# Kernel tuning notes

Hardware: AMD Instinct MI355X
Metric: run time of the kernel (lower is better)

The kernel has to match this reference:

```python
import jax, jax.numpy as jnp
import numpy as np

MODES = 16
WIDTH = 64
SCHMIDT = 8
N_LAYERS = 4


def _spectral_conv(x, wr, wi, modes):
    """Quantum spectral conv: truncated 2D FFT -> complex Schmidt-rank einsum -> inverse FFT.
    x: (B,H,W,C) real. wr, wi: (modes,modes,C,C,S)."""
    b, H, W, C = x.shape
    S = wr.shape[-1]
    # quantum_fourier_modes: keep low (modes x modes) Fourier modes
    x_ft = jnp.fft.fftn(x, axes=(1, 2))[:, :modes, :modes, :]          # (B,m,n,C) complex
    w = wr + 1j * wi                                                     # (m,n,C,C,S)
    # tensor_product_einsum('b...nc,mncos->b...mos')
    out_ft = jnp.einsum('bxnc,mncos->bxmos', x_ft, w)                   # (B,m,m,C,S)
    # recombine Schmidt components (normalized sum over rank)
    out_ft = out_ft.sum(axis=-1) * (1.0 / float(np.sqrt(S)))            # (B,m,m,C)
    full = jnp.zeros((b, H, W, C), dtype=x_ft.dtype).at[:, :modes, :modes, :].set(out_ft)
    # inverse quantum_fourier_modes + .real
    return jnp.fft.ifftn(full, axes=(1, 2)).real


def setup_inputs() -> dict:
    key = jax.random.key(0)
    ks = jax.random.split(key, 12)
    B, H, W, Cin = 16, 128, 128, 3
    sc = 0.02
    inp = {
        'x': jax.random.normal(ks[0], (B, H, W, Cin), jnp.float32),
        'fc_in_w': jax.random.normal(ks[1], (Cin, WIDTH), jnp.float32) * sc,
        'fc_in_b': jnp.zeros((WIDTH,), jnp.float32),
        'wr': jax.random.normal(ks[2], (N_LAYERS, MODES, MODES, WIDTH, WIDTH, SCHMIDT), jnp.float32) * sc,
        'wi': jax.random.normal(ks[3], (N_LAYERS, MODES, MODES, WIDTH, WIDTH, SCHMIDT), jnp.float32) * sc,
        'ww': jax.random.normal(ks[4], (N_LAYERS, WIDTH, WIDTH), jnp.float32) * sc,
        'wb': jnp.zeros((N_LAYERS, WIDTH), jnp.float32),
        'fc1_w': jax.random.normal(ks[5], (WIDTH, 128), jnp.float32) * sc,
        'fc1_b': jnp.zeros((128,), jnp.float32),
        'fc2_w': jax.random.normal(ks[6], (128, 1), jnp.float32) * sc,
        'fc2_b': jnp.zeros((1,), jnp.float32),
    }
    return inp


def reference(x, fc_in_w, fc_in_b, wr, wi, ww, wb, fc1_w, fc1_b, fc2_w, fc2_b) -> jnp.ndarray:
    h = x @ fc_in_w + fc_in_b                                   # (B,H,W,width)
    for i in range(N_LAYERS):
        x1 = _spectral_conv(h, wr[i], wi[i], MODES)             # quantum spectral path
        x2 = h @ ww[i] + wb[i]                                  # pointwise Dense path
        h = jax.nn.gelu(x1 + x2)
    h = jax.nn.gelu(h @ fc1_w + fc1_b)
    return h @ fc2_w + fc2_b                                    # (B,H,W,1)
```

## Files before the change

### kernel.cpp

```cpp
#include <hip/hip_runtime.h>
#include <math.h>


#define TWO_PI_128 0.049087385212340517f

__device__ __forceinline__ float gelu_f(float v) {
  float ex = 1.5957691216057308f * v * fmaf(0.044715f, v * v, 1.0f);
  float e = __expf(fminf(ex, 30.0f));
  float r = __builtin_amdgcn_rcpf(e + 1.0f);
  return fmaf(-v, r, v);
}

__global__ __launch_bounds__(256) void k_fc_in(const float* __restrict__ x,
    const float* __restrict__ w, const float* __restrict__ b,
    float* __restrict__ h) {
  int t = blockIdx.x * 256 + threadIdx.x;
  int pix = t >> 4, c4 = (t & 15) << 2;
  float x0 = x[pix * 3], x1 = x[pix * 3 + 1], x2 = x[pix * 3 + 2];
  float4 acc = *(const float4*)&b[c4];
  float4 w0 = *(const float4*)&w[c4];
  float4 w1 = *(const float4*)&w[64 + c4];
  float4 w2 = *(const float4*)&w[128 + c4];
  acc.x = fmaf(x2, w2.x, fmaf(x1, w1.x, fmaf(x0, w0.x, acc.x)));
  acc.y = fmaf(x2, w2.y, fmaf(x1, w1.y, fmaf(x0, w0.y, acc.y)));
  acc.z = fmaf(x2, w2.z, fmaf(x1, w1.z, fmaf(x0, w0.z, acc.z)));
  acc.w = fmaf(x2, w2.w, fmaf(x1, w1.w, fmaf(x0, w0.w, acc.w)));
  *(float4*)&h[(size_t)pix * 64 + c4] = acc;
}

__global__ __launch_bounds__(256) void k_prep(const float* __restrict__ wr,
    const float* __restrict__ wi, float* __restrict__ Br, float* __restrict__ Bi) {
  int t = blockIdx.x * 256 + threadIdx.x;
  int o = t & 63, c = (t >> 6) & 63, n = (t >> 12) & 15, m = t >> 16;
  const float4* pr = (const float4*)(wr) + (size_t)t * 2;
  float4 a = pr[0], d = pr[1];
  float sr = ((a.x + a.y) + (a.z + a.w)) + ((d.x + d.y) + (d.z + d.w));
  const float4* pi = (const float4*)(wi) + (size_t)t * 2;
  a = pi[0]; d = pi[1];
  float si = ((a.x + a.y) + (a.z + a.w)) + ((d.x + d.y) + (d.z + d.w));
  const float scale = 0.35355339059327373f / 16384.0f;
  int k = n * 64 + c, j = m * 64 + o;
  Br[k * 1024 + j] = sr * scale;
  Bi[k * 1024 + j] = si * scale;
}

__global__ __launch_bounds__(256) void k_dft_y(const float* __restrict__ h,
                                               float2* __restrict__ A1) {
  __shared__ float sh[128 * 64];
  int bx = blockIdx.x;
  const float* src = h + (size_t)bx * 8192;
  for (int i = threadIdx.x; i < 2048; i += 256)
    *(float4*)&sh[i * 4] = *(const float4*)&src[i * 4];
  __syncthreads();
  int c = threadIdx.x & 63, kg = threadIdx.x >> 6;
  float s4r[4][4], s4i[4][4];
  float w4r[4], w4i[4], c4t[4], s4t[4];
  #pragma unroll
  for (int q = 0; q < 4; ++q) {
    int ky = kg + 4 * q;
    __sincosf(-TWO_PI_128 * 4.0f * (float)ky, &s4t[q], &c4t[q]);
    w4r[q] = 1.f; w4i[q] = 0.f;
    #pragma unroll
    for (int p = 0; p < 4; ++p) { s4r[q][p] = 0.f; s4i[q][p] = 0.f; }
  }
  for (int m = 0; m < 32; ++m) {
    float hv[4];
    #pragma unroll
    for (int p = 0; p < 4; ++p) hv[p] = sh[(4 * m + p) * 64 + c];
    #pragma unroll
    for (int q = 0; q < 4; ++q) {
      #pragma unroll
      for (int p = 0; p < 4; ++p) {
        s4r[q][p] = fmaf(hv[p], w4r[q], s4r[q][p]);
        s4i[q][p] = fmaf(hv[p], w4i[q], s4i[q][p]);
      }
      float nw = w4r[q] * c4t[q] - w4i[q] * s4t[q];
      w4i[q] = fmaf(w4i[q], c4t[q], w4r[q] * s4t[q]);
      w4r[q] = nw;
    }
  }
  #pragma unroll
  for (int q = 0; q < 4; ++q) {
    int ky = kg + 4 * q;
    float s1, c1;
    __sincosf(-TWO_PI_128 * (float)ky, &s1, &c1);
    float sr = s4r[q][0], si = s4i[q][0];
    float wr_ = c1, wi_ = s1;
    #pragma unroll
    for (int p = 1; p < 4; ++p) {
      sr = fmaf(s4r[q][p], wr_, sr); sr = fmaf(-s4i[q][p], wi_, sr);
      si = fmaf(s4r[q][p], wi_, si); si = fmaf(s4i[q][p], wr_, si);
      float nw = wr_ * c1 - wi_ * s1;
      wi_ = fmaf(wi_, c1, wr_ * s1);
      wr_ = nw;
    }
    A1[((size_t)bx * 16 + ky) * 64 + c] = make_float2(sr, si);
  }
}

__global__ __launch_bounds__(256) void k_dft_x(const float2* __restrict__ A1,
    float* __restrict__ Ar, float* __restrict__ Ai) {
  __shared__ float2 sh[128 * 32];
  int b = blockIdx.x, ky = blockIdx.y, ch = blockIdx.z;
  int c0 = ch * 32;
  for (int i = threadIdx.x; i < 2048; i += 256) {
    int xx = i >> 4, u = (i & 15) * 2;
    *(float4*)&sh[xx * 32 + u] =
        *(const float4*)&A1[(((size_t)b * 128 + xx) * 16 + ky) * 64 + c0 + u];
  }
  __syncthreads();
  int cl = threadIdx.x & 31, kxg = threadIdx.x >> 5;
  float cs[2], sn[2], wr_[2], wi_[2], sr[2], si[2];
  #pragma unroll
  for (int q = 0; q < 2; ++q) {
    int kx = kxg + 8 * q;
    __sincosf(-TWO_PI_128 * (float)kx, &sn[q], &cs[q]);
    wr_[q] = 1.f; wi_[q] = 0.f; sr[q] = 0.f; si[q] = 0.f;
  }
  for (int xx = 0; xx < 128; ++xx) {
    float2 v = sh[xx * 32 + cl];
    #pragma unroll
    for (int q = 0; q < 2; ++q) {
      sr[q] = fmaf(v.x, wr_[q], sr[q]); sr[q] = fmaf(-v.y, wi_[q], sr[q]);
      si[q] = fmaf(v.x, wi_[q], si[q]); si[q] = fmaf(v.y, wr_[q], si[q]);
      float nw = wr_[q] * cs[q] - wi_[q] * sn[q];
      wi_[q] = fmaf(wi_[q], cs[q], wr_[q] * sn[q]);
      wr_[q] = nw;
    }
  }
  #pragma unroll
  for (int q = 0; q < 2; ++q) {
    int kx = kxg + 8 * q;
    int row = b * 16 + kx, col = ky * 64 + c0 + cl;
    Ar[row * 1024 + col] = sr[q];
    Ai[row * 1024 + col] = si[q];
  }
}

#define CMAC(cr, ci, ax, ay, bx, by)                 \
  cr = fmaf(ax, bx, cr); cr = fmaf(-(ay), by, cr);   \
  ci = fmaf(ax, by, ci); ci = fmaf(ay, bx, ci);

__global__ __launch_bounds__(256) void k_gemm(const float* __restrict__ Ar,
    const float* __restrict__ Ai, const float* __restrict__ Br,
    const float* __restrict__ Bi, float2* __restrict__ Cp,
    float2* __restrict__ Pp) {
  __shared__ float2 As[2][64][34];
  __shared__ float2 Bs[2][32][66];
  int t = threadIdx.x;
  int tx = t & 15, ty = t >> 4;
  int col0 = blockIdx.x * 64, row0 = blockIdx.y * 64, kb0 = blockIdx.z * 128;
  int ra = t >> 2, ka8 = (t & 3) * 8;
  int rb = t >> 3, jb8 = (t & 7) * 8;
  float4 arv0, arv1, aiv0, aiv1, brv0, brv1, biv0, biv1;
  float cr[4][4] = {{0,0,0,0},{0,0,0,0},{0,0,0,0},{0,0,0,0}};
  float ci[4][4] = {{0,0,0,0},{0,0,0,0},{0,0,0,0},{0,0,0,0}};

  auto ldT = [&](int k0) {
    int g = (row0 + ra) * 1024 + k0 + ka8;
    arv0 = *(const float4*)&Ar[g]; arv1 = *(const float4*)&Ar[g + 4];
    aiv0 = *(const float4*)&Ai[g]; aiv1 = *(const float4*)&Ai[g + 4];
    int gb = (k0 + rb) * 1024 + col0 + jb8;
    brv0 = *(const float4*)&Br[gb]; brv1 = *(const float4*)&Br[gb + 4];
    biv0 = *(const float4*)&Bi[gb]; biv1 = *(const float4*)&Bi[gb + 4];
  };
  auto stT = [&](int buf) {
    *(float4*)&As[buf][ra][ka8]     = make_float4(arv0.x, aiv0.x, arv0.y, aiv0.y);
    *(float4*)&As[buf][ra][ka8 + 2] = make_float4(arv0.z, aiv0.z, arv0.w, aiv0.w);
    *(float4*)&As[buf][ra][ka8 + 4] = make_float4(arv1.x, aiv1.x, arv1.y, aiv1.y);
    *(float4*)&As[buf][ra][ka8 + 6] = make_float4(arv1.z, aiv1.z, arv1.w, aiv1.w);
    *(float4*)&Bs[buf][rb][jb8]     = make_float4(brv0.x, biv0.x, brv0.y, biv0.y);
    *(float4*)&Bs[buf][rb][jb8 + 2] = make_float4(brv0.z, biv0.z, brv0.w, biv0.w);
    *(float4*)&Bs[buf][rb][jb8 + 4] = make_float4(brv1.x, biv1.x, brv1.y, biv1.y);
    *(float4*)&Bs[buf][rb][jb8 + 6] = make_float4(brv1.z, biv1.z, brv1.w, biv1.w);
  };

  ldT(kb0); stT(0);
  __syncthreads();
  for (int kt = 0; kt < 4; ++kt) {
    if (kt < 3) ldT(kb0 + (kt + 1) * 32);
    int cur = kt & 1;
    #pragma unroll 4
    for (int kk2 = 0; kk2 < 16; ++kk2) {
      float4 av[4];
      #pragma unroll
      for (int rr = 0; rr < 4; ++rr)
        av[rr] = *(const float4*)&As[cur][ty * 4 + rr][kk2 * 2];
      float2 b0[4], b1[4];
      #pragma unroll
      for (int jj = 0; jj < 4; ++jj) b0[jj] = Bs[cur][kk2 * 2][tx + jj * 16];
      #pragma unroll
      for (int jj = 0; jj < 4; ++jj) b1[jj] = Bs[cur][kk2 * 2 + 1][tx + jj * 16];
      #pragma unroll
      for (int rr = 0; rr < 4; ++rr) {
        #pragma unroll
        for (int jj = 0; jj < 4; ++jj) {
          CMAC(cr[rr][jj], ci[rr][jj], av[rr].x, av[rr].y, b0[jj].x, b0[jj].y)
          CMAC(cr[rr][jj], ci[rr][jj], av[rr].z, av[rr].w, b1[jj].x, b1[jj].y)
        }
      }
    }
    if (kt < 3) stT(cur ^ 1);
    __syncthreads();
  }
  float2* Co = (blockIdx.z == 0) ? Cp : Pp + (size_t)(blockIdx.z - 1) * 262144;
  #pragma unroll
  for (int rr = 0; rr < 4; ++rr) {
    int r = row0 + ty * 4 + rr;
    #pragma unroll
    for (int jj = 0; jj < 4; ++jj) {
      int j = col0 + tx + jj * 16;
      Co[(size_t)r * 1024 + j] = make_float2(cr[rr][jj], ci[rr][jj]);
    }
  }
}

__global__ __launch_bounds__(256) void k_csum(float2* __restrict__ Cp,
                                              const float2* __restrict__ Pp) {
  int i = blockIdx.x * 256 + threadIdx.x;
  float4* c0 = (float4*)Cp;
  float4 s = c0[i];
  #pragma unroll
  for (int z = 0; z < 7; ++z) {
    float4 v = ((const float4*)(Pp + (size_t)z * 262144))[i];
    s.x += v.x; s.y += v.y; s.z += v.z; s.w += v.w;
  }
  c0[i] = s;
}

__global__ __launch_bounds__(256) void k_ifft_y(const float2* __restrict__ Cp,
                                                float2* __restrict__ T) {
  __shared__ float2 Cl[1024];
  int b = blockIdx.x >> 4, kx = blockIdx.x & 15;
  int row = b * 16 + kx;
  for (int i = threadIdx.x; i < 512; i += 256)
    *(float4*)&Cl[i * 2] = *(const float4*)&Cp[(size_t)row * 1024 + i * 2];
  __syncthreads();
  int c = threadIdx.x & 63, yg = threadIdx.x >> 6;
  for (int y = yg; y < 128; y += 4) {
    float snv, csv;
    __sincosf(TWO_PI_128 * (float)y, &snv, &csv);
    float wr_ = 1.f, wi_ = 0.f, sr = 0.f, si = 0.f;
    #pragma unroll
    for (int ky = 0; ky < 16; ++ky) {
      float2 v = Cl[ky * 64 + c];
      sr = fmaf(v.x, wr_, sr); sr = fmaf(-v.y, wi_, sr);
      si = fmaf(v.x, wi_, si); si = fmaf(v.y, wr_, si);
      float nw = wr_ * csv - wi_ * snv;
      wi_ = fmaf(wi_, csv, wr_ * snv);
      wr_ = nw;
    }
    T[(((size_t)b * 128 + y) * 16 + kx) * 64 + c] = make_float2(sr, si);
  }
}

__global__ __launch_bounds__(256, 4) void k_layer_out(const float* hin,
    const float2* __restrict__ T, const float* __restrict__ ww,
    const float* __restrict__ wb, float* hout) {
  __shared__ alignas(16) float wwT[64 * 68];
  __shared__ alignas(16) float2 Tl[1024];
  int b = blockIdx.x >> 7, y = blockIdx.x & 127;
  for (int i = threadIdx.x; i < 1024; i += 256) {
    int k = i >> 4, c4 = (i & 15) << 2;
    float4 v = *(const float4*)&ww[k * 64 + c4];
    wwT[(c4 + 0) * 68 + k] = v.x;
    wwT[(c4 + 1) * 68 + k] = v.y;
    wwT[(c4 + 2) * 68 + k] = v.z;
    wwT[(c4 + 3) * 68 + k] = v.w;
  }
  const float2* Tp = T + ((size_t)b * 128 + y) * 1024;
  for (int i = threadIdx.x; i < 512; i += 256)
    *(float4*)&Tl[i * 2] = *(const float4*)&Tp[i * 2];
  __syncthreads();
  int ct = threadIdx.x & 7, xg = threadIdx.x >> 3;
  float acc[4][8];
  #pragma unroll
  for (int cc = 0; cc < 8; ++cc) {
    float bv = wb[ct + 8 * cc];
    #pragma unroll
    for (int j = 0; j < 4; ++j) acc[j][cc] = bv;
  }
  #pragma unroll
  for (int kx = 0; kx < 16; ++kx) {
    float tr[8], ti[8];
    #pragma unroll
    for (int cc = 0; cc < 8; ++cc) {
      float2 v = Tl[kx * 64 + ct + 8 * cc];
      tr[cc] = v.x; ti[cc] = v.y;
    }
    float s0v, c0v;
    __sincosf(TWO_PI_128 * (float)(kx * xg), &s0v, &c0v);
    float wr_ = c0v, wi_ = s0v;
    #pragma unroll
    for (int j = 0; j < 4; ++j) {
      #pragma unroll
      for (int cc = 0; cc < 8; ++cc) {
        acc[j][cc] = fmaf(tr[cc], wr_, acc[j][cc]);
        acc[j][cc] = fmaf(-ti[cc], wi_, acc[j][cc]);
      }
      float owr = wr_, owi = wi_;
      if ((kx & 3) == 1)      { wr_ = -owi; wi_ =  owr; }
      else if ((kx & 3) == 2) { wr_ = -owr; wi_ = -owi; }
      else if ((kx & 3) == 3) { wr_ =  owi; wi_ = -owr; }
    }
  }
  const float* hp = hin + (((size_t)b * 128 + xg) * 128 + y) * 64;
  #pragma unroll 1
  for (int kq = 0; kq < 64; kq += 4) {
    float4 wv[8];
    #pragma unroll
    for (int cc = 0; cc < 8; ++cc)
      wv[cc] = *(const float4*)&wwT[(ct + 8 * cc) * 68 + kq];
    #pragma unroll
    for (int j = 0; j < 4; ++j) {
      float4 hv = *(const float4*)&hp[(size_t)j * 262144 + kq];
      #pragma unroll
      for (int cc = 0; cc < 8; ++cc) {
        acc[j][cc] = fmaf(hv.x, wv[cc].x, acc[j][cc]);
        acc[j][cc] = fmaf(hv.y, wv[cc].y, acc[j][cc]);
        acc[j][cc] = fmaf(hv.z, wv[cc].z, acc[j][cc]);
        acc[j][cc] = fmaf(hv.w, wv[cc].w, acc[j][cc]);
      }
    }
  }
  __syncthreads();
  #pragma unroll
  for (int j = 0; j < 4; ++j) {
    int xx = xg + 32 * j;
    size_t base = (((size_t)b * 128 + xx) * 128 + y) * 64 + ct;
    #pragma unroll
    for (int cc = 0; cc < 8; ++cc)
      hout[base + 8 * cc] = gelu_f(acc[j][cc]);
  }
}

__global__ __launch_bounds__(256) void k_final(const float* __restrict__ h,
    const float* __restrict__ w1, const float* __restrict__ b1,
    const float* __restrict__ w2, const float* __restrict__ b2,
    float* __restrict__ out) {
  __shared__ alignas(16) float w1T[128 * 68];
  __shared__ alignas(16) float hl[128 * 68];
  __shared__ float b1s[128];
  __shared__ float w2s[128];
  for (int i = threadIdx.x; i < 8192; i += 256) {
    int k = i >> 7, j = i & 127;
    w1T[j * 68 + k] = w1[i];
  }
  if (threadIdx.x < 128) {
    b1s[threadIdx.x] = b1[threadIdx.x];
    w2s[threadIdx.x] = w2[threadIdx.x];
  }
  int r0 = blockIdx.x * 128;
  for (int i = threadIdx.x; i < 2048; i += 256) {
    int r = i >> 4, kq = (i & 15) * 4;
    float4 v = *(const float4*)&h[(size_t)(r0 + r) * 64 + kq];
    *(float4*)&hl[r * 68 + kq] = v;
  }
  __syncthreads();
  int jt = threadIdx.x & 15, rg = threadIdx.x >> 4;
  float acc[8][8];
  #pragma unroll
  for (int cc = 0; cc < 8; ++cc) {
    float bv = b1s[jt + 16 * cc];
    #pragma unroll
    for (int ii = 0; ii < 8; ++ii) acc[ii][cc] = bv;
  }
  #pragma unroll 1
  for (int kq = 0; kq < 64; kq += 4) {
    float4 hv[8];
    #pragma unroll
    for (int ii = 0; ii < 8; ++ii)
      hv[ii] = *(const float4*)&hl[(rg + 16 * ii) * 68 + kq];
    #pragma unroll
    for (int cc = 0; cc < 8; ++cc) {
      float4 wv = *(const float4*)&w1T[(jt + 16 * cc) * 68 + kq];
      #pragma unroll
      for (int ii = 0; ii < 8; ++ii) {
        acc[ii][cc] = fmaf(hv[ii].x, wv.x, acc[ii][cc]);
        acc[ii][cc] = fmaf(hv[ii].y, wv.y, acc[ii][cc]);
        acc[ii][cc] = fmaf(hv[ii].z, wv.z, acc[ii][cc]);
        acc[ii][cc] = fmaf(hv[ii].w, wv.w, acc[ii][cc]);
      }
    }
  }
  float b2v = b2[0];
  #pragma unroll
  for (int ii = 0; ii < 8; ++ii) {
    float part = 0.f;
    #pragma unroll
    for (int cc = 0; cc < 8; ++cc)
      part = fmaf(gelu_f(acc[ii][cc]), w2s[jt + 16 * cc], part);
    part += __shfl_xor(part, 1, 64);
    part += __shfl_xor(part, 2, 64);
    part += __shfl_xor(part, 4, 64);
    part += __shfl_xor(part, 8, 64);
    if (jt == 0) out[r0 + rg + 16 * ii] = part + b2v;
  }
}

extern "C" void kernel_launch(void* const* d_in, const int* in_sizes, int n_in,
                              void* d_out, int out_size, void* d_ws, size_t ws_size,
                              hipStream_t stream) {
  (void)in_sizes; (void)n_in; (void)out_size; (void)ws_size;
  const float* x      = (const float*)d_in[0];
  const float* fcin_w = (const float*)d_in[1];
  const float* fcin_b = (const float*)d_in[2];
  const float* wr     = (const float*)d_in[3];
  const float* wi     = (const float*)d_in[4];
  const float* ww     = (const float*)d_in[5];
  const float* wb     = (const float*)d_in[6];
  const float* fc1_w  = (const float*)d_in[7];
  const float* fc1_b  = (const float*)d_in[8];
  const float* fc2_w  = (const float*)d_in[9];
  const float* fc2_b  = (const float*)d_in[10];
  float* out = (float*)d_out;

  float*  hA = (float*)d_ws;
  float2* A1 = (float2*)(hA + 16777216);
  float*  Ar = (float*)(A1 + 2097152);
  float*  Ai = Ar + 262144;
  float*  Br = Ai + 262144;
  float*  Bi = Br + 1048576;
  float2* Cp = (float2*)(Bi + 1048576);

  k_fc_in<<<16384, 256, 0, stream>>>(x, fcin_w, fcin_b, hA);
  for (int l = 0; l < 4; ++l) {
    k_prep<<<4096, 256, 0, stream>>>(wr + (size_t)l * 8388608,
                                     wi + (size_t)l * 8388608, Br, Bi);
    k_dft_y<<<2048, 256, 0, stream>>>(hA, A1);
    k_dft_x<<<dim3(16, 16, 2), 256, 0, stream>>>(A1, Ar, Ai);
    k_gemm<<<dim3(16, 4, 8), 256, 0, stream>>>(Ar, Ai, Br, Bi, Cp, A1);
    k_csum<<<512, 256, 0, stream>>>(Cp, A1);
    k_ifft_y<<<256, 256, 0, stream>>>(Cp, A1);
    k_layer_out<<<2048, 256, 0, stream>>>(hA, A1, ww + (size_t)l * 4096,
                                          wb + (size_t)l * 64, hA);
  }
  k_final<<<2048, 256, 0, stream>>>(hA, fc1_w, fc1_b, fc2_w, fc2_b, out);
}
```

Before: 964.5 us.

## Replace FP32 complex GEMM with split-bf16 MFMA GEMM and fold partial sum

Replaces the FP32 CUDA-core complex GEMM with an MFMA bf16 GEMM. Each operand is split into high and low bf16 parts, and three products per real product are kept to approximate fp32 accuracy. New split kernels convert A and B into an MFMA-friendly packed layout. The split-K is reduced from 8 to 2, and the remaining partial sum moves into the ifft_y load, which removes the csum kernel. This adds conversion passes and extra memory traffic in exchange, and it loses some precision compared with full fp32.

```diff
diff --git a/kernel.cpp b/kernel.cpp
--- a/kernel.cpp
+++ b/kernel.cpp
@@ -3,12 +3,22 @@
 
 
 #define TWO_PI_128 0.049087385212340517f
+
+typedef __attribute__((ext_vector_type(8))) short bf16x8;
+typedef __attribute__((ext_vector_type(4))) float f32x4;
 
 __device__ __forceinline__ float gelu_f(float v) {
   float ex = 1.5957691216057308f * v * fmaf(0.044715f, v * v, 1.0f);
   float e = __expf(fminf(ex, 30.0f));
   float r = __builtin_amdgcn_rcpf(e + 1.0f);
   return fmaf(-v, r, v);
+}
+
+__device__ __forceinline__ ushort bf16_rne(float v, float& back) {
+  uint u = __float_as_uint(v);
+  uint r = (u + 0x7FFFu + ((u >> 16) & 1u)) >> 16;
+  back = __uint_as_float(r << 16);
+  return (ushort)r;
 }
 
 __global__ __launch_bounds__(256) void k_fc_in(const float* __restrict__ x,
@@ -137,104 +147,118 @@
   }
 }
 
-#define CMAC(cr, ci, ax, ay, bx, by)                 \
-  cr = fmaf(ax, bx, cr); cr = fmaf(-(ay), by, cr);   \
-  ci = fmaf(ax, by, ci); ci = fmaf(ay, bx, ci);
-
-__global__ __launch_bounds__(256) void k_gemm(const float* __restrict__ Ar,
-    const float* __restrict__ Ai, const float* __restrict__ Br,
-    const float* __restrict__ Bi, float2* __restrict__ Cp,
-    float2* __restrict__ Pp) {
-  __shared__ float2 As[2][64][34];
-  __shared__ float2 Bs[2][32][66];
-  int t = threadIdx.x;
-  int tx = t & 15, ty = t >> 4;
-  int col0 = blockIdx.x * 64, row0 = blockIdx.y * 64, kb0 = blockIdx.z * 128;
-  int ra = t >> 2, ka8 = (t & 3) * 8;
-  int rb = t >> 3, jb8 = (t & 7) * 8;
-  float4 arv0, arv1, aiv0, aiv1, brv0, brv1, biv0, biv1;
-  float cr[4][4] = {{0,0,0,0},{0,0,0,0},{0,0,0,0},{0,0,0,0}};
-  float ci[4][4] = {{0,0,0,0},{0,0,0,0},{0,0,0,0},{0,0,0,0}};
-
-  auto ldT = [&](int k0) {
-    int g = (row0 + ra) * 1024 + k0 + ka8;
-    arv0 = *(const float4*)&Ar[g]; arv1 = *(const float4*)&Ar[g + 4];
-    aiv0 = *(const float4*)&Ai[g]; aiv1 = *(const float4*)&Ai[g + 4];
-    int gb = (k0 + rb) * 1024 + col0 + jb8;
-    brv0 = *(const float4*)&Br[gb]; brv1 = *(const float4*)&Br[gb + 4];
-    biv0 = *(const float4*)&Bi[gb]; biv1 = *(const float4*)&Bi[gb + 4];
+__global__ __launch_bounds__(256) void k_asplit(const float* __restrict__ Ar,
+    const float* __restrict__ Ai, ushort* __restrict__ Ap) {
+  int g = blockIdx.x * 256 + threadIdx.x;
+  size_t off = (size_t)g * 8;
+  float4 r0 = *(const float4*)&Ar[off], r1 = *(const float4*)&Ar[off + 4];
+  float4 i0 = *(const float4*)&Ai[off], i1 = *(const float4*)&Ai[off + 4];
+  float vr[8] = {r0.x, r0.y, r0.z, r0.w, r1.x, r1.y, r1.z, r1.w};
+  float vi[8] = {i0.x, i0.y, i0.z, i0.w, i1.x, i1.y, i1.z, i1.w};
+  ushort hr[8], lr[8], hi_[8], li[8];
+  #pragma unroll
+  for (int j = 0; j < 8; ++j) {
+    float back, d;
+    hr[j] = bf16_rne(vr[j], back);
+    lr[j] = bf16_rne(vr[j] - back, d);
+    hi_[j] = bf16_rne(vi[j], back);
+    li[j] = bf16_rne(vi[j] - back, d);
+  }
+  auto pack = [](const ushort* s) {
+    return make_uint4((uint)s[0] | ((uint)s[1] << 16), (uint)s[2] | ((uint)s[3] << 16),
+                      (uint)s[4] | ((uint)s[5] << 16), (uint)s[6] | ((uint)s[7] << 16));
   };
-  auto stT = [&](int buf) {
-    *(float4*)&As[buf][ra][ka8]     = make_float4(arv0.x, aiv0.x, arv0.y, aiv0.y);
-    *(float4*)&As[buf][ra][ka8 + 2] = make_float4(arv0.z, aiv0.z, arv0.w, aiv0.w);
-    *(float4*)&As[buf][ra][ka8 + 4] = make_float4(arv1.x, aiv1.x, arv1.y, aiv1.y);
-    *(float4*)&As[buf][ra][ka8 + 6] = make_float4(arv1.z, aiv1.z, arv1.w, aiv1.w);
-    *(float4*)&Bs[buf][rb][jb8]     = make_float4(brv0.x, biv0.x, brv0.y, biv0.y);
-    *(float4*)&Bs[buf][rb][jb8 + 2] = make_float4(brv0.z, biv0.z, brv0.w, biv0.w);
-    *(float4*)&Bs[buf][rb][jb8 + 4] = make_float4(brv1.x, biv1.x, brv1.y, biv1.y);
-    *(float4*)&Bs[buf][rb][jb8 + 6] = make_float4(brv1.z, biv1.z, brv1.w, biv1.w);
+  *(uint4*)(Ap + 0 * 262144 + off) = pack(hr);
+  *(uint4*)(Ap + 1 * 262144 + off) = pack(lr);
+  *(uint4*)(Ap + 2 * 262144 + off) = pack(hi_);
+  *(uint4*)(Ap + 3 * 262144 + off) = pack(li);
+}
+
+__global__ __launch_bounds__(256) void k_bsplit(const float* __restrict__ Br,
+    const float* __restrict__ Bi, ushort* __restrict__ Bf) {
+  int t = blockIdx.x * 256 + threadIdx.x;
+  int l = t & 63, ks = (t >> 6) & 31, nt = t >> 11;
+  int col = nt * 16 + (l & 15);
+  int kb = ks * 32 + (l >> 4) * 8;
+  ushort hr[8], lr[8], hi_[8], li[8];
+  #pragma unroll
+  for (int j = 0; j < 8; ++j) {
+    float vr = Br[(size_t)(kb + j) * 1024 + col];
+    float vi = Bi[(size_t)(kb + j) * 1024 + col];
+    float back, d;
+    hr[j] = bf16_rne(vr, back);
+    lr[j] = bf16_rne(vr - back, d);
+    hi_[j] = bf16_rne(vi, back);
+    li[j] = bf16_rne(vi - back, d);
+  }
+  auto pack = [](const ushort* s) {
+    return make_uint4((uint)s[0] | ((uint)s[1] << 16), (uint)s[2] | ((uint)s[3] << 16),
+                      (uint)s[4] | ((uint)s[5] << 16), (uint)s[6] | ((uint)s[7] << 16));
   };
-
-  ldT(kb0); stT(0);
-  __syncthreads();
-  for (int kt = 0; kt < 4; ++kt) {
-    if (kt < 3) ldT(kb0 + (kt + 1) * 32);
-    int cur = kt & 1;
-    #pragma unroll 4
-    for (int kk2 = 0; kk2 < 16; ++kk2) {
-      float4 av[4];
-      #pragma unroll
-      for (int rr = 0; rr < 4; ++rr)
-        av[rr] = *(const float4*)&As[cur][ty * 4 + rr][kk2 * 2];
-      float2 b0[4], b1[4];
-      #pragma unroll
-      for (int jj = 0; jj < 4; ++jj) b0[jj] = Bs[cur][kk2 * 2][tx + jj * 16];
-      #pragma unroll
-      for (int jj = 0; jj < 4; ++jj) b1[jj] = Bs[cur][kk2 * 2 + 1][tx + jj * 16];
-      #pragma unroll
-      for (int rr = 0; rr < 4; ++rr) {
-        #pragma unroll
-        for (int jj = 0; jj < 4; ++jj) {
-          CMAC(cr[rr][jj], ci[rr][jj], av[rr].x, av[rr].y, b0[jj].x, b0[jj].y)
-          CMAC(cr[rr][jj], ci[rr][jj], av[rr].z, av[rr].w, b1[jj].x, b1[jj].y)
-        }
-      }
-    }
-    if (kt < 3) stT(cur ^ 1);
-    __syncthreads();
-  }
-  float2* Co = (blockIdx.z == 0) ? Cp : Pp + (size_t)(blockIdx.z - 1) * 262144;
-  #pragma unroll
-  for (int rr = 0; rr < 4; ++rr) {
-    int r = row0 + ty * 4 + rr;
-    #pragma unroll
-    for (int jj = 0; jj < 4; ++jj) {
-      int j = col0 + tx + jj * 16;
-      Co[(size_t)r * 1024 + j] = make_float2(cr[rr][jj], ci[rr][jj]);
-    }
-  }
-}
-
-__global__ __launch_bounds__(256) void k_csum(float2* __restrict__ Cp,
-                                              const float2* __restrict__ Pp) {
-  int i = blockIdx.x * 256 + threadIdx.x;
-  float4* c0 = (float4*)Cp;
-  float4 s = c0[i];
-  #pragma unroll
-  for (int z = 0; z < 7; ++z) {
-    float4 v = ((const float4*)(Pp + (size_t)z * 262144))[i];
-    s.x += v.x; s.y += v.y; s.z += v.z; s.w += v.w;
-  }
-  c0[i] = s;
+  size_t off = (size_t)t * 8;
+  *(uint4*)(Bf + 0 * 1048576 + off) = pack(hr);
+  *(uint4*)(Bf + 1 * 1048576 + off) = pack(lr);
+  *(uint4*)(Bf + 2 * 1048576 + off) = pack(hi_);
+  *(uint4*)(Bf + 3 * 1048576 + off) = pack(li);
+}
+
+__global__ __launch_bounds__(256) void k_gemm_mfma(const ushort* __restrict__ Ap,
+    const ushort* __restrict__ Bf, float2* __restrict__ Cp,
+    float2* __restrict__ Pz1) {
+  int wid = threadIdx.x >> 6, l = threadIdx.x & 63;
+  int bid = blockIdx.x;
+  int z = bid & 1;
+  int tile = (bid >> 1) * 4 + wid;
+  int tr = tile & 15, tc = tile >> 4;
+  int r0 = tr * 16;
+  int lr = l & 15, lk = l >> 4;
+  size_t aoff = (size_t)(r0 + lr) * 1024 + z * 512 + lk * 8;
+  size_t boff = (((size_t)tc * 32 + z * 16) * 64 + l) * 8;
+  f32x4 rr = {0,0,0,0}, ii = {0,0,0,0}, ri = {0,0,0,0}, ir = {0,0,0,0};
+  #pragma unroll 4
+  for (int ks = 0; ks < 16; ++ks) {
+    bf16x8 arH = *(const bf16x8*)(Ap + 0 * 262144 + aoff);
+    bf16x8 arL = *(const bf16x8*)(Ap + 1 * 262144 + aoff);
+    bf16x8 aiH = *(const bf16x8*)(Ap + 2 * 262144 + aoff);
+    bf16x8 aiL = *(const bf16x8*)(Ap + 3 * 262144 + aoff);
+    bf16x8 brH = *(const bf16x8*)(Bf + 0 * 1048576 + boff);
+    bf16x8 brL = *(const bf16x8*)(Bf + 1 * 1048576 + boff);
+    bf16x8 biH = *(const bf16x8*)(Bf + 2 * 1048576 + boff);
+    bf16x8 biL = *(const bf16x8*)(Bf + 3 * 1048576 + boff);
+    rr = __builtin_amdgcn_mfma_f32_16x16x32_bf16(arH, brH, rr, 0, 0, 0);
+    rr = __builtin_amdgcn_mfma_f32_16x16x32_bf16(arH, brL, rr, 0, 0, 0);
+    rr = __builtin_amdgcn_mfma_f32_16x16x32_bf16(arL, brH, rr, 0, 0, 0);
+    ii = __builtin_amdgcn_mfma_f32_16x16x32_bf16(aiH, biH, ii, 0, 0, 0);
+    ii = __builtin_amdgcn_mfma_f32_16x16x32_bf16(aiH, biL, ii, 0, 0, 0);
+    ii = __builtin_amdgcn_mfma_f32_16x16x32_bf16(aiL, biH, ii, 0, 0, 0);
+    ri = __builtin_amdgcn_mfma_f32_16x16x32_bf16(arH, biH, ri, 0, 0, 0);
+    ri = __builtin_amdgcn_mfma_f32_16x16x32_bf16(arH, biL, ri, 0, 0, 0);
+    ri = __builtin_amdgcn_mfma_f32_16x16x32_bf16(arL, biH, ri, 0, 0, 0);
+    ir = __builtin_amdgcn_mfma_f32_16x16x32_bf16(aiH, brH, ir, 0, 0, 0);
+    ir = __builtin_amdgcn_mfma_f32_16x16x32_bf16(aiH, brL, ir, 0, 0, 0);
+    ir = __builtin_amdgcn_mfma_f32_16x16x32_bf16(aiL, brH, ir, 0, 0, 0);
+    aoff += 32;
+    boff += 512;
+  }
+  float2* Co = z ? Pz1 : Cp;
+  int col = tc * 16 + lr;
+  #pragma unroll
+  for (int q = 0; q < 4; ++q) {
+    int row = r0 + lk * 4 + q;
+    Co[(size_t)row * 1024 + col] = make_float2(rr[q] - ii[q], ri[q] + ir[q]);
+  }
 }
 
 __global__ __launch_bounds__(256) void k_ifft_y(const float2* __restrict__ Cp,
-                                                float2* __restrict__ T) {
+    const float2* __restrict__ P1, float2* __restrict__ T) {
   __shared__ float2 Cl[1024];
   int b = blockIdx.x >> 4, kx = blockIdx.x & 15;
   int row = b * 16 + kx;
-  for (int i = threadIdx.x; i < 512; i += 256)
-    *(float4*)&Cl[i * 2] = *(const float4*)&Cp[(size_t)row * 1024 + i * 2];
+  for (int i = threadIdx.x; i < 512; i += 256) {
+    float4 u = *(const float4*)&Cp[(size_t)row * 1024 + i * 2];
+    float4 v = *(const float4*)&P1[(size_t)row * 1024 + i * 2];
+    *(float4*)&Cl[i * 2] = make_float4(u.x + v.x, u.y + v.y, u.z + v.z, u.w + v.w);
+  }
   __syncthreads();
   int c = threadIdx.x & 63, yg = threadIdx.x >> 6;
   for (int y = yg; y < 128; y += 4) {
@@ -422,6 +446,9 @@
   float*  Br = Ai + 262144;
   float*  Bi = Br + 1048576;
   float2* Cp = (float2*)(Bi + 1048576);
+  ushort* Bf = (ushort*)A1;
+  ushort* Ap = Bf + 4 * 1048576;
+  float2* Pz1 = (float2*)Ar;
 
   k_fc_in<<<16384, 256, 0, stream>>>(x, fcin_w, fcin_b, hA);
   for (int l = 0; l < 4; ++l) {
@@ -429,9 +456,10 @@
                                      wi + (size_t)l * 8388608, Br, Bi);
     k_dft_y<<<2048, 256, 0, stream>>>(hA, A1);
     k_dft_x<<<dim3(16, 16, 2), 256, 0, stream>>>(A1, Ar, Ai);
-    k_gemm<<<dim3(16, 4, 8), 256, 0, stream>>>(Ar, Ai, Br, Bi, Cp, A1);
-    k_csum<<<512, 256, 0, stream>>>(Cp, A1);
-    k_ifft_y<<<256, 256, 0, stream>>>(Cp, A1);
+    k_asplit<<<128, 256, 0, stream>>>(Ar, Ai, Ap);
+    k_bsplit<<<512, 256, 0, stream>>>(Br, Bi, Bf);
+    k_gemm_mfma<<<512, 256, 0, stream>>>(Ap, Bf, Cp, Pz1);
+    k_ifft_y<<<256, 256, 0, stream>>>(Cp, Pz1, A1);
     k_layer_out<<<2048, 256, 0, stream>>>(hA, A1, ww + (size_t)l * 4096,
                                           wb + (size_t)l * 64, hA);
   }
```

Measured after the change: 942.3 us. 1.02x faster.
